# Kernel optimization log

Hardware: AMD Instinct MI355X
Metric: run time of the kernel (lower is better)

Reference implementation:

```python
import jax, jax.numpy as jnp
import numpy as np

B, CIN, COUT, HIN = 2, 64, 64, 96
ALPHA = 0.2       # LeakyReLU slope in GAT
K_RANK = 6        # dist.argsort(1).argsort(1) <= 6  -> 7 nearest neighbors incl. self
DN = ('NCHW', 'OIHW', 'NCHW')


def setup_inputs():
    key = jax.random.key(0)
    ks = jax.random.split(key, 10)
    sc = lambda k, shape, s: jax.random.normal(k, shape, jnp.float32) * s
    return {
        'x': jax.random.normal(ks[0], (B, CIN, HIN, HIN), jnp.float32),
        'conv_w': sc(ks[1], (COUT, CIN, 3, 3), 0.05),
        'conv_b': jnp.zeros((COUT,), jnp.float32),
        'W1': sc(ks[2], (COUT, COUT), 0.1),
        'a1': sc(ks[3], (2 * COUT,), 0.1),
        'W2': sc(ks[4], (COUT, COUT), 0.1),
        'a2': sc(ks[5], (2 * COUT,), 0.1),
        'Wout': sc(ks[6], (2 * COUT, COUT), 0.1),
        'aout': sc(ks[7], (2 * COUT,), 0.1),
        'tconv_w': sc(ks[8], (COUT, COUT, 3, 3), 0.05),  # torch ConvTranspose2d layout [in,out,kh,kw]
        'tconv_b': jnp.zeros((COUT,), jnp.float32),
    }


def _gat_layer(h, adj, W, a, concat):
    # h: [B,N,F_in], W: [F_in,F_out], a: [2*F_out]
    Wh = h @ W                                   # [B,N,F']
    Fo = W.shape[1]
    e = (Wh @ a[:Fo])[:, :, None] + (Wh @ a[Fo:])[:, None, :]   # [B,N,N]
    e = jax.nn.leaky_relu(e, ALPHA)
    e = jnp.where(adj > 0, e, -9e15)
    attn = jax.nn.softmax(e, axis=-1)
    out = jnp.einsum('bij,bjf->bif', attn, Wh)
    return jax.nn.elu(out) if concat else out


def reference(x, conv_w, conv_b, W1, a1, W2, a2, Wout, aout, tconv_w, tconv_b):
    # --- Pre_ProcessLayer_Graph: stride-2 conv, flatten, 7-NN dense adjacency ---
    y = jax.lax.conv_general_dilated(x, conv_w, (2, 2), ((1, 1), (1, 1)),
                                     dimension_numbers=DN) + conv_b[None, :, None, None]
    Bb, C, H, W_ = y.shape
    N = H * W_
    feat = y.reshape(Bb, C, N).transpose(0, 2, 1)          # [B,N,C]
    sq = jnp.sum(feat * feat, axis=-1)                     # [B,N]
    d2 = sq[:, :, None] + sq[:, None, :] - 2.0 * jnp.einsum('bic,bjc->bij', feat, feat)
    dist = jnp.sqrt(jnp.maximum(d2, 0.0))                  # euclidean cdist
    ranks = jnp.argsort(jnp.argsort(dist, axis=-1), axis=-1)
    adj = (ranks <= K_RANK).astype(feat.dtype)             # [B,N,N] binary, incl. self (rank 0)
    # --- GAT (pyGAT style): 2 concat heads + output attention layer, eval mode ---
    h1 = _gat_layer(feat, adj, W1, a1, True)
    h2 = _gat_layer(feat, adj, W2, a2, True)
    hcat = jnp.concatenate([h1, h2], axis=-1)              # [B,N,2C]
    g = jax.nn.elu(_gat_layer(hcat, adj, Wout, aout, False))  # [B,N,C]
    # --- reshape back + transpose conv (k=3, s=2, p=1, output_padding=1) ---
    g = g.transpose(0, 2, 1).reshape(Bb, C, H, W_)
    wt = jnp.flip(tconv_w, (2, 3)).transpose(1, 0, 2, 3)   # -> [out,in,kh,kw]
    out = jax.lax.conv_general_dilated(g, wt, (1, 1), ((1, 2), (1, 2)),
                                       lhs_dilation=(2, 2),
                                       dimension_numbers=DN) + tconv_b[None, :, None, None]
    return out
```

## Files before the change

### kernel.cpp

```cpp
#include <hip/hip_runtime.h>
#include <hip/hip_bf16.h>
#include <stdint.h>

using bf16 = __hip_bfloat16;
using u64 = unsigned long long;

constexpr int B_ = 2;
constexpr int N_ = 2304;

constexpr int OFF_WC2   = 0;
constexpr int OFF_WT2   = 36864;
constexpr int OFF_W1F   = 73728;
constexpr int OFF_W2F   = 77824;
constexpr int OFF_WOUTF = 81920;
constexpr int OFF_A1F   = 90112;
constexpr int OFF_A2F   = 90240;
constexpr int OFF_AOUTF = 90368;
constexpr int OFF_CBF   = 90496;
constexpr int OFF_TBF   = 90560;
constexpr int OFF_FLAG  = 90624;
constexpr int OFF_SQ    = 90688;
constexpr int OFF_S11   = 95296;
constexpr int OFF_S12   = 99904;
constexpr int OFF_S21   = 104512;
constexpr int OFF_S22   = 109120;
constexpr int OFF_S1O   = 113728;
constexpr int OFF_S2O   = 118336;
constexpr int OFF_KNN   = 122944;
constexpr int OFF_BUF0  = 159808;
constexpr int OFF_BUF1  = 454720;
constexpr int OFF_BUF2  = 749632;
constexpr int OFF_BUF3  = 1044544;
constexpr int OFF_PK    = 1339456;

__device__ __forceinline__ float bf2f_raw(unsigned short u) {
    return __uint_as_float(((unsigned int)u) << 16);
}

__device__ __forceinline__ unsigned int mono32(float f) {
    unsigned int u = __float_as_uint(f);
    return (u & 0x80000000u) ? ~u : (u | 0x80000000u);
}

__device__ __forceinline__ bool detect_f32(const void* conv_w) {
    const unsigned short* cw = (const unsigned short*)conv_w;
    float m = 0.f;
    #pragma unroll
    for (int u = 0; u < 64; ++u) {
        float v = fabsf(bf2f_raw(cw[u]));
        if (v < 3.0e38f) m = fmaxf(m, v);
    }
    return m > 1.0e4f;
}

__global__ __launch_bounds__(256) void kc_prep(
    const void* conv_w, const void* conv_b, const void* W1, const void* a1,
    const void* W2, const void* a2, const void* Wout, const void* aout,
    const void* tconv_w, const void* tconv_b, float* __restrict__ ws)
{
    bool f32 = detect_f32(conv_w);
    int idx = blockIdx.x * 256 + threadIdx.x;
    if (idx == 0) ws[OFF_FLAG] = f32 ? 1.f : 0.f;
    if (idx < 32256) ws[OFF_SQ + idx] = 0.f;

    {
        int tap = idx >> 12, ic = (idx >> 6) & 63, oc = idx & 63;
        if (f32) {
            ws[OFF_WC2 + idx] = ((const float*)conv_w)[(oc * 64 + ic) * 9 + tap];
            ws[OFF_WT2 + idx] = ((const float*)tconv_w)[(ic * 64 + oc) * 9 + tap];
        } else {
            ws[OFF_WC2 + idx] = bf2f_raw(((const unsigned short*)conv_w)[(oc * 64 + ic) * 9 + tap]);
            ws[OFF_WT2 + idx] = bf2f_raw(((const unsigned short*)tconv_w)[(ic * 64 + oc) * 9 + tap]);
        }
    }
    if (idx < 4096) {
        if (f32) {
            ws[OFF_W1F + idx] = ((const float*)W1)[idx];
            ws[OFF_W2F + idx] = ((const float*)W2)[idx];
        } else {
            ws[OFF_W1F + idx] = bf2f_raw(((const unsigned short*)W1)[idx]);
            ws[OFF_W2F + idx] = bf2f_raw(((const unsigned short*)W2)[idx]);
        }
    }
    if (idx < 8192)
        ws[OFF_WOUTF + idx] = f32 ? ((const float*)Wout)[idx]
                                  : bf2f_raw(((const unsigned short*)Wout)[idx]);
    if (idx < 128) {
        if (f32) {
            ws[OFF_A1F + idx]   = ((const float*)a1)[idx];
            ws[OFF_A2F + idx]   = ((const float*)a2)[idx];
            ws[OFF_AOUTF + idx] = ((const float*)aout)[idx];
        } else {
            ws[OFF_A1F + idx]   = bf2f_raw(((const unsigned short*)a1)[idx]);
            ws[OFF_A2F + idx]   = bf2f_raw(((const unsigned short*)a2)[idx]);
            ws[OFF_AOUTF + idx] = bf2f_raw(((const unsigned short*)aout)[idx]);
        }
    }
    if (idx < 64) {
        if (f32) {
            ws[OFF_CBF + idx] = ((const float*)conv_b)[idx];
            ws[OFF_TBF + idx] = ((const float*)tconv_b)[idx];
        } else {
            ws[OFF_CBF + idx] = bf2f_raw(((const unsigned short*)conv_b)[idx]);
            ws[OFF_TBF + idx] = bf2f_raw(((const unsigned short*)tconv_b)[idx]);
        }
    }
}

template <bool F32>
__device__ __forceinline__ void conv_body(const void* __restrict__ x,
                                          float* __restrict__ ws,
                                          int n, int ocb, int b)
{
    int oy = n / 48, ox = n - (n / 48) * 48;
    const float* wc2 = ws + OFF_WC2;
    size_t xb = (size_t)b * 64 * 9216;
    float acc[4] = {0, 0, 0, 0};

    for (int ky = 0; ky < 3; ++ky) {
        int iy = 2 * oy - 1 + ky;
        bool vy = (unsigned)iy < 96u;
        int iyc = vy ? iy : 0;
        for (int kx = 0; kx < 3; ++kx) {
            int ix = 2 * ox - 1 + kx;
            bool v = vy && ((unsigned)ix < 96u);
            int ixc = v ? ix : 0;
            size_t xoff = xb + iyc * 96 + ixc;
            const float* wb = wc2 + (ky * 3 + kx) * 4096 + ocb;
            #pragma unroll 8
            for (int ic = 0; ic < 64; ++ic) {
                float xv;
                if (F32) xv = ((const float*)x)[xoff + ic * 9216];
                else     xv = bf2f_raw(((const unsigned short*)x)[xoff + ic * 9216]);
                xv = v ? xv : 0.f;
                const float* wr = wb + ic * 64;
                #pragma unroll
                for (int o = 0; o < 4; ++o) acc[o] += xv * wr[o];
            }
        }
    }
    float* featT = ws + OFF_BUF0 + (size_t)b * 64 * N_;
    const float* cb = ws + OFF_CBF;
    float ssum = 0.f;
    #pragma unroll
    for (int o = 0; o < 4; ++o) {
        float f = acc[o] + cb[ocb + o];
        acc[o] = f;
        featT[(ocb + o) * N_ + n] = f;
        ssum += f * f;
    }
    *(float4*)(ws + OFF_BUF2 + ((size_t)(b * N_ + n) * 64 + ocb)) =
        make_float4(acc[0], acc[1], acc[2], acc[3]);
    atomicAdd(ws + OFF_SQ + b * N_ + n, ssum);
}

__global__ __launch_bounds__(128) void k1_conv(const void* __restrict__ x,
                                               float* __restrict__ ws)
{
    int n   = blockIdx.x * 128 + threadIdx.x;
    int ocb = blockIdx.y * 4;
    int b   = blockIdx.z;
    if (ws[OFF_FLAG] != 0.f) conv_body<true >(x, ws, n, ocb, b);
    else                     conv_body<false>(x, ws, n, ocb, b);
}

__global__ __launch_bounds__(256) void k2_knn(float* __restrict__ ws)
{
    __shared__ float Bs[32][256];
    __shared__ float ys[32][260];
    int tid = threadIdx.x;
    int i0  = blockIdx.x * 32;
    int jh  = blockIdx.y;
    int b   = i0 / N_;
    const float* fT  = ws + OFF_BUF0 + (size_t)b * 64 * N_;
    const float* fnc = ws + OFF_BUF2;
    const float* sq  = ws + OFF_SQ + b * N_;
    int w = tid >> 6, lane = tid & 63;
    int r0 = w * 8;
    int arow0 = __builtin_amdgcn_readfirstlane(i0 + r0);

    u64 K[7];
    #pragma unroll
    for (int t = 0; t < 7; ++t) K[t] = ~0ull;

    int rsel = r0 + (lane >> 3);
    int g    = lane & 7;

    for (int jt = 0; jt < 3; ++jt) {
        int jb = jh * 768 + jt * 256;
        float acc[8][4];
        #pragma unroll
        for (int r = 0; r < 8; ++r)
            #pragma unroll
            for (int c = 0; c < 4; ++c) acc[r][c] = 0.f;

        for (int kh = 0; kh < 2; ++kh) {
            __syncthreads();
            #pragma unroll
            for (int it = 0; it < 8; ++it) {
                int idx = tid + it * 256;
                int k = idx >> 6, j4 = idx & 63;
                float4 v = *(const float4*)(fT + (size_t)(kh * 32 + k) * N_ + jb + j4 * 4);
                *(float4*)&Bs[k][j4 * 4] = v;
            }
            __syncthreads();

            #pragma unroll 2
            for (int k4 = 0; k4 < 8; ++k4) {
                float4 Bv[4];
                #pragma unroll
                for (int kk = 0; kk < 4; ++kk)
                    Bv[kk] = *(const float4*)&Bs[k4 * 4 + kk][4 * lane];
                #pragma unroll
                for (int r = 0; r < 8; ++r) {
                    float4 a = *(const float4*)(fnc + (size_t)(arow0 + r) * 64
                                                + kh * 32 + k4 * 4);
                    acc[r][0] += a.x * Bv[0].x + a.y * Bv[1].x + a.z * Bv[2].x + a.w * Bv[3].x;
                    acc[r][1] += a.x * Bv[0].y + a.y * Bv[1].y + a.z * Bv[2].y + a.w * Bv[3].y;
                    acc[r][2] += a.x * Bv[0].z + a.y * Bv[1].z + a.z * Bv[2].z + a.w * Bv[3].z;
                    acc[r][3] += a.x * Bv[0].w + a.y * Bv[1].w + a.z * Bv[2].w + a.w * Bv[3].w;
                }
            }
        }

        float4 sqv = *(const float4*)(sq + jb + 4 * lane);
        #pragma unroll
        for (int r = 0; r < 8; ++r) {
            float4 yv;
            yv.x = sqv.x - 2.f * acc[r][0];
            yv.y = sqv.y - 2.f * acc[r][1];
            yv.z = sqv.z - 2.f * acc[r][2];
            yv.w = sqv.w - 2.f * acc[r][3];
            *(float4*)&ys[r0 + r][4 * lane] = yv;
        }

        #pragma unroll 8
        for (int u = 0; u < 32; ++u) {
            int jl = g + 8 * u;
            float y = ys[rsel][jl];
            u64 key = ((u64)mono32(y) << 32) | (unsigned int)(jb + jl);
            if (key < K[6]) {
                int pos = 0;
                #pragma unroll
                for (int s = 0; s < 7; ++s) pos += (K[s] < key) ? 1 : 0;
                #pragma unroll
                for (int p = 6; p > 0; --p)
                    K[p] = (p == pos) ? key : ((p > pos) ? K[p - 1] : K[p]);
                if (pos == 0) K[0] = key;
            }
        }
        __syncthreads();
    }

    u64 myk = 0;
    for (int pass = 0; pass < 7; ++pass) {
        u64 m = K[0];
        #pragma unroll
        for (int s = 1; s < 7; ++s) m = (K[s] < m) ? K[s] : m;
        #pragma unroll
        for (int off = 1; off < 8; off <<= 1) {
            u64 o = (u64)__shfl_xor((long long)m, off);
            m = (o < m) ? o : m;
        }
        #pragma unroll
        for (int s = 0; s < 7; ++s)
            if (K[s] == m) K[s] = ~0ull;
        if (g == pass) myk = m;
    }
    if (g < 7) {
        u64* pk = (u64*)(ws + OFF_PK);
        pk[((size_t)(i0 + rsel) * 3 + jh) * 8 + g] = myk;
    }
}

__global__ __launch_bounds__(256) void k_lin(float* __restrict__ ws)
{
    int g = blockIdx.y;
    if (g == 32) {
        int row = blockIdx.x * 256 + threadIdx.x;
        const u64* pk = (const u64*)(ws + OFF_PK) + (size_t)row * 24;
        int* kout = (int*)(ws + OFF_KNN) + (size_t)row * 8;
        u64 L0[7], L1[7], L2[7];
        #pragma unroll
        for (int q = 0; q < 7; ++q) { L0[q] = pk[q]; L1[q] = pk[8 + q]; L2[q] = pk[16 + q]; }
        #pragma unroll
        for (int q = 0; q < 7; ++q) {
            int rank = q;
            #pragma unroll
            for (int p = 0; p < 7; ++p)
                rank += ((L1[p] < L0[q]) ? 1 : 0) + ((L2[p] < L0[q]) ? 1 : 0);
            if (rank < 7) kout[rank] = (int)(L0[q] & 0xffffffffull);
        }
        #pragma unroll
        for (int q = 0; q < 7; ++q) {
            int rank = q;
            #pragma unroll
            for (int p = 0; p < 7; ++p)
                rank += ((L0[p] < L1[q]) ? 1 : 0) + ((L2[p] < L1[q]) ? 1 : 0);
            if (rank < 7) kout[rank] = (int)(L1[q] & 0xffffffffull);
        }
        #pragma unroll
        for (int q = 0; q < 7; ++q) {
            int rank = q;
            #pragma unroll
            for (int p = 0; p < 7; ++p)
                rank += ((L0[p] < L2[q]) ? 1 : 0) + ((L1[p] < L2[q]) ? 1 : 0);
            if (rank < 7) kout[rank] = (int)(L2[q] & 0xffffffffull);
        }
        return;
    }
    int layer = g >> 4;
    int ocb = (g & 15) * 4;
    const float* W  = ws + (layer ? OFF_W2F : OFF_W1F);
    const float* a  = ws + (layer ? OFF_A2F : OFF_A1F);
    float* out_nc   = ws + (layer ? OFF_BUF3 : OFF_BUF1);
    float* s1       = ws + (layer ? OFF_S21 : OFF_S11);
    float* s2       = ws + (layer ? OFF_S22 : OFF_S12);
    int i = blockIdx.x * 256 + threadIdx.x;
    int b = i / N_, n = i - b * N_;
    const float* in_b = ws + OFF_BUF0 + (size_t)b * 64 * N_;

    float acc[4] = {0, 0, 0, 0};
    #pragma unroll 8
    for (int kk = 0; kk < 64; ++kk) {
        float xv = in_b[kk * N_ + n];
        const float* wr = W + kk * 64 + ocb;
        #pragma unroll
        for (int o = 0; o < 4; ++o) acc[o] += xv * wr[o];
    }
    *(float4*)(out_nc + ((size_t)i * 64 + ocb)) =
        make_float4(acc[0], acc[1], acc[2], acc[3]);
    float p1 = 0.f, p2 = 0.f;
    #pragma unroll
    for (int o = 0; o < 4; ++o) {
        p1 += acc[o] * a[ocb + o];
        p2 += acc[o] * a[64 + ocb + o];
    }
    atomicAdd(s1 + i, p1);
    atomicAdd(s2 + i, p2);
}

__global__ __launch_bounds__(256) void k_lin2(float* __restrict__ ws)
{
    int ocb = blockIdx.y * 4;
    int i = blockIdx.x * 256 + threadIdx.x;
    int b = i / N_, n = i - b * N_;
    const float* h1 = ws + OFF_BUF2 + (size_t)b * 64 * N_;
    const float* h2 = ws + OFF_BUF0 + (size_t)b * 64 * N_;
    const float* W  = ws + OFF_WOUTF;
    const float* a  = ws + OFF_AOUTF;

    float acc[4] = {0, 0, 0, 0};
    #pragma unroll 8
    for (int kk = 0; kk < 64; ++kk) {
        float xv = h1[kk * N_ + n];
        const float* wr = W + kk * 64 + ocb;
        #pragma unroll
        for (int o = 0; o < 4; ++o) acc[o] += xv * wr[o];
    }
    #pragma unroll 8
    for (int kk = 0; kk < 64; ++kk) {
        float xv = h2[kk * N_ + n];
        const float* wr = W + (64 + kk) * 64 + ocb;
        #pragma unroll
        for (int o = 0; o < 4; ++o) acc[o] += xv * wr[o];
    }
    *(float4*)(ws + OFF_BUF1 + ((size_t)i * 64 + ocb)) =
        make_float4(acc[0], acc[1], acc[2], acc[3]);
    float p1 = 0.f, p2 = 0.f;
    #pragma unroll
    for (int o = 0; o < 4; ++o) {
        p1 += acc[o] * a[ocb + o];
        p2 += acc[o] * a[64 + ocb + o];
    }
    atomicAdd(ws + OFF_S1O + i, p1);
    atomicAdd(ws + OFF_S2O + i, p2);
}

__device__ __forceinline__ void attn_body(
    const float* __restrict__ Wh_nc, const float* __restrict__ s1,
    const float* __restrict__ s2, const int* __restrict__ knn,
    float* __restrict__ out, int i, int b, int n, int c4)
{
    const int* kp = knn + (size_t)i * 8;
    int j[7];
    #pragma unroll
    for (int t = 0; t < 7; ++t) {
        int jt = kp[t];
        j[t] = ((unsigned)jt < (unsigned)N_) ? jt : 0;
    }
    float si = s1[i];
    const float* s2b = s2 + b * N_;
    float e[7];
    #pragma unroll
    for (int t = 0; t < 7; ++t) {
        float v = si + s2b[j[t]];
        e[t] = v > 0.f ? v : 0.2f * v;
    }
    float m = e[0];
    #pragma unroll
    for (int t = 1; t < 7; ++t) m = fmaxf(m, e[t]);
    float ssum = 0.f;
    #pragma unroll
    for (int t = 0; t < 7; ++t) { e[t] = __expf(e[t] - m); ssum += e[t]; }
    float inv = 1.f / ssum;
    #pragma unroll
    for (int t = 0; t < 7; ++t) e[t] *= inv;

    const float4* W4 = (const float4*)Wh_nc;
    float4 acc = make_float4(0.f, 0.f, 0.f, 0.f);
    #pragma unroll
    for (int t = 0; t < 7; ++t) {
        float4 v = W4[(size_t)(b * N_ + j[t]) * 16 + c4];
        acc.x += e[t] * v.x; acc.y += e[t] * v.y;
        acc.z += e[t] * v.z; acc.w += e[t] * v.w;
    }
    acc.x = acc.x > 0.f ? acc.x : expm1f(acc.x);
    acc.y = acc.y > 0.f ? acc.y : expm1f(acc.y);
    acc.z = acc.z > 0.f ? acc.z : expm1f(acc.z);
    acc.w = acc.w > 0.f ? acc.w : expm1f(acc.w);
    float* ob = out + (size_t)b * 64 * N_;
    ob[(c4 * 4 + 0) * N_ + n] = acc.x;
    ob[(c4 * 4 + 1) * N_ + n] = acc.y;
    ob[(c4 * 4 + 2) * N_ + n] = acc.z;
    ob[(c4 * 4 + 3) * N_ + n] = acc.w;
}

__global__ __launch_bounds__(256) void k_attn12(float* __restrict__ ws)
{
    int layer = blockIdx.z;
    const float* Wh_nc = ws + (layer ? OFF_BUF3 : OFF_BUF1);
    const float* s1    = ws + (layer ? OFF_S21 : OFF_S11);
    const float* s2    = ws + (layer ? OFF_S22 : OFF_S12);
    float* out         = ws + (layer ? OFF_BUF0 : OFF_BUF2);
    int c4 = blockIdx.y;
    int i = blockIdx.x * 256 + threadIdx.x;
    int b = i / N_, n = i - b * N_;
    attn_body(Wh_nc, s1, s2, (const int*)(ws + OFF_KNN), out, i, b, n, c4);
}

__global__ __launch_bounds__(256) void k_attn_out(float* __restrict__ ws)
{
    int c4 = blockIdx.y;
    int i = blockIdx.x * 256 + threadIdx.x;
    int b = i / N_, n = i - b * N_;
    attn_body(ws + OFF_BUF1, ws + OFF_S1O, ws + OFF_S2O,
              (const int*)(ws + OFF_KNN), ws + OFF_BUF3, i, b, n, c4);
}

__global__ __launch_bounds__(128) void k7_tconv(float* __restrict__ ws,
                                                void* __restrict__ outp)
{
    bool f32 = ws[OFF_FLAG] != 0.f;
    int pixc = blockIdx.x * 128 + threadIdx.x;
    int g    = blockIdx.y;
    int pc   = g >> 3, ocb = (g & 7) * 8;
    int b    = blockIdx.z;
    int py = pc >> 1, px = pc & 1;
    int ay = pixc / 48, bx = pixc - (pixc / 48) * 48;
    int oy = 2 * ay + py, ox = 2 * bx + px;

    const float* gT  = ws + OFF_BUF3 + (size_t)b * 64 * N_;
    const float* wt2 = ws + OFF_WT2;
    float acc[8] = {0, 0, 0, 0, 0, 0, 0, 0};

    int nky = py ? 2 : 1;
    int nkx = px ? 2 : 1;
    for (int s = 0; s < nky; ++s) {
        int ky = py ? (s == 0 ? 0 : 2) : 1;
        int iy = py ? (s == 0 ? ay + 1 : ay) : ay;
        bool vy = iy < 48;
        for (int t = 0; t < nkx; ++t) {
            int kx = px ? (t == 0 ? 0 : 2) : 1;
            int ix = px ? (t == 0 ? bx + 1 : bx) : bx;
            bool v = vy && (ix < 48);
            const float* gp = gT + (v ? iy * 48 + ix : 0);
            const float* wb = wt2 + (ky * 3 + kx) * 4096 + ocb;
            #pragma unroll 8
            for (int ic = 0; ic < 64; ++ic) {
                float gv = gp[ic * N_];
                gv = v ? gv : 0.f;
                const float* wr = wb + ic * 64;
                #pragma unroll
                for (int o = 0; o < 8; ++o) acc[o] += gv * wr[o];
            }
        }
    }
    const float* tb = ws + OFF_TBF;
    size_t base = ((size_t)(b * 64 + ocb) * 96 + oy) * 96 + ox;
    if (f32) {
        float* op = (float*)outp;
        #pragma unroll
        for (int o = 0; o < 8; ++o) op[base + (size_t)o * 9216] = acc[o] + tb[ocb + o];
    } else {
        bf16* op = (bf16*)outp;
        #pragma unroll
        for (int o = 0; o < 8; ++o)
            op[base + (size_t)o * 9216] = __float2bfloat16(acc[o] + tb[ocb + o]);
    }
}

extern "C" void kernel_launch(void* const* d_in, const int* in_sizes, int n_in,
                              void* d_out, int out_size, void* d_ws, size_t ws_size,
                              hipStream_t stream)
{
    float* ws = (float*)d_ws;

    hipLaunchKernelGGL(kc_prep, dim3(144), dim3(256), 0, stream,
                       d_in[1], d_in[2], d_in[3], d_in[4], d_in[5], d_in[6],
                       d_in[7], d_in[8], d_in[9], d_in[10], ws);
    hipLaunchKernelGGL(k1_conv, dim3(18, 16, 2), dim3(128), 0, stream, d_in[0], ws);
    hipLaunchKernelGGL(k2_knn, dim3(144, 3), dim3(256), 0, stream, ws);
    hipLaunchKernelGGL(k_lin, dim3(18, 33), dim3(256), 0, stream, ws);
    hipLaunchKernelGGL(k_attn12, dim3(18, 16, 2), dim3(256), 0, stream, ws);
    hipLaunchKernelGGL(k_lin2, dim3(18, 16), dim3(256), 0, stream, ws);
    hipLaunchKernelGGL(k_attn_out, dim3(18, 16), dim3(256), 0, stream, ws);
    hipLaunchKernelGGL(k7_tconv, dim3(18, 32, 2), dim3(128), 0, stream, ws, d_out);
}
```

Baseline: 238.1 us.

## Fuse all stages into one persistent kernel with software grid barriers

Replaces the eight separate kernel launches with a single persistent kernel of 432 blocks. The blocks step through prep, conv, kNN, linear, attention and transposed-conv phases, separated by an atomic-counter grid barrier, and a memset resets the barrier first. This removes per-launch overhead and inter-kernel gaps. It also re-tiles several phases: the kNN y-tile is split into halves so shared memory fits at three blocks per CU, and the attention and tconv phases each handle more channels per thread. In exchange, phases with little work leave blocks idle at barriers, and correctness depends on all 432 blocks being resident at the same time.

```diff
diff --git a/kernel.cpp b/kernel.cpp
--- a/kernel.cpp
+++ b/kernel.cpp
@@ -5,8 +5,9 @@
 using bf16 = __hip_bfloat16;
 using u64 = unsigned long long;
 
-constexpr int B_ = 2;
-constexpr int N_ = 2304;
+constexpr int B_   = 2;
+constexpr int N_   = 2304;
+constexpr int NBLK = 432;
 
 constexpr int OFF_WC2   = 0;
 constexpr int OFF_WT2   = 36864;
@@ -18,7 +19,7 @@
 constexpr int OFF_AOUTF = 90368;
 constexpr int OFF_CBF   = 90496;
 constexpr int OFF_TBF   = 90560;
-constexpr int OFF_FLAG  = 90624;
+constexpr int OFF_BAR   = 90624;
 constexpr int OFF_SQ    = 90688;
 constexpr int OFF_S11   = 95296;
 constexpr int OFF_S12   = 99904;
@@ -53,58 +54,24 @@
     return m > 1.0e4f;
 }
 
-__global__ __launch_bounds__(256) void kc_prep(
-    const void* conv_w, const void* conv_b, const void* W1, const void* a1,
-    const void* W2, const void* a2, const void* Wout, const void* aout,
-    const void* tconv_w, const void* tconv_b, float* __restrict__ ws)
+__device__ __forceinline__ void gbar(int* bar)
 {
-    bool f32 = detect_f32(conv_w);
-    int idx = blockIdx.x * 256 + threadIdx.x;
-    if (idx == 0) ws[OFF_FLAG] = f32 ? 1.f : 0.f;
-    if (idx < 32256) ws[OFF_SQ + idx] = 0.f;
-
-    {
-        int tap = idx >> 12, ic = (idx >> 6) & 63, oc = idx & 63;
-        if (f32) {
-            ws[OFF_WC2 + idx] = ((const float*)conv_w)[(oc * 64 + ic) * 9 + tap];
-            ws[OFF_WT2 + idx] = ((const float*)tconv_w)[(ic * 64 + oc) * 9 + tap];
+    __syncthreads();
+    if (threadIdx.x == 0) {
+        __threadfence();
+        int gen = atomicAdd(&bar[1], 0);
+        int old = atomicAdd(&bar[0], 1);
+        if (old == NBLK - 1) {
+            bar[0] = 0;
+            __threadfence();
+            atomicAdd(&bar[1], 1);
         } else {
-            ws[OFF_WC2 + idx] = bf2f_raw(((const unsigned short*)conv_w)[(oc * 64 + ic) * 9 + tap]);
-            ws[OFF_WT2 + idx] = bf2f_raw(((const unsigned short*)tconv_w)[(ic * 64 + oc) * 9 + tap]);
-        }
-    }
-    if (idx < 4096) {
-        if (f32) {
-            ws[OFF_W1F + idx] = ((const float*)W1)[idx];
-            ws[OFF_W2F + idx] = ((const float*)W2)[idx];
-        } else {
-            ws[OFF_W1F + idx] = bf2f_raw(((const unsigned short*)W1)[idx]);
-            ws[OFF_W2F + idx] = bf2f_raw(((const unsigned short*)W2)[idx]);
-        }
-    }
-    if (idx < 8192)
-        ws[OFF_WOUTF + idx] = f32 ? ((const float*)Wout)[idx]
-                                  : bf2f_raw(((const unsigned short*)Wout)[idx]);
-    if (idx < 128) {
-        if (f32) {
-            ws[OFF_A1F + idx]   = ((const float*)a1)[idx];
-            ws[OFF_A2F + idx]   = ((const float*)a2)[idx];
-            ws[OFF_AOUTF + idx] = ((const float*)aout)[idx];
-        } else {
-            ws[OFF_A1F + idx]   = bf2f_raw(((const unsigned short*)a1)[idx]);
-            ws[OFF_A2F + idx]   = bf2f_raw(((const unsigned short*)a2)[idx]);
-            ws[OFF_AOUTF + idx] = bf2f_raw(((const unsigned short*)aout)[idx]);
-        }
-    }
-    if (idx < 64) {
-        if (f32) {
-            ws[OFF_CBF + idx] = ((const float*)conv_b)[idx];
-            ws[OFF_TBF + idx] = ((const float*)tconv_b)[idx];
-        } else {
-            ws[OFF_CBF + idx] = bf2f_raw(((const unsigned short*)conv_b)[idx]);
-            ws[OFF_TBF + idx] = bf2f_raw(((const unsigned short*)tconv_b)[idx]);
-        }
-    }
+            while (atomicAdd(&bar[1], 0) == gen)
+                __builtin_amdgcn_s_sleep(8);
+        }
+        __threadfence();
+    }
+    __syncthreads();
 }
 
 template <bool F32>
@@ -154,130 +121,278 @@
     atomicAdd(ws + OFF_SQ + b * N_ + n, ssum);
 }
 
-__global__ __launch_bounds__(128) void k1_conv(const void* __restrict__ x,
-                                               float* __restrict__ ws)
+__device__ __forceinline__ void attn_body8(
+    const float* __restrict__ Wh_nc, const float* __restrict__ s1,
+    const float* __restrict__ s2, const int* __restrict__ knn,
+    float* __restrict__ out, int i, int b, int n, int c8)
 {
-    int n   = blockIdx.x * 128 + threadIdx.x;
-    int ocb = blockIdx.y * 4;
-    int b   = blockIdx.z;
-    if (ws[OFF_FLAG] != 0.f) conv_body<true >(x, ws, n, ocb, b);
-    else                     conv_body<false>(x, ws, n, ocb, b);
-}
-
-__global__ __launch_bounds__(256) void k2_knn(float* __restrict__ ws)
+    const int* kp = knn + (size_t)i * 8;
+    int j[7];
+    #pragma unroll
+    for (int t = 0; t < 7; ++t) {
+        int jt = kp[t];
+        j[t] = ((unsigned)jt < (unsigned)N_) ? jt : 0;
+    }
+    float si = s1[i];
+    const float* s2b = s2 + b * N_;
+    float e[7];
+    #pragma unroll
+    for (int t = 0; t < 7; ++t) {
+        float v = si + s2b[j[t]];
+        e[t] = v > 0.f ? v : 0.2f * v;
+    }
+    float m = e[0];
+    #pragma unroll
+    for (int t = 1; t < 7; ++t) m = fmaxf(m, e[t]);
+    float ssum = 0.f;
+    #pragma unroll
+    for (int t = 0; t < 7; ++t) { e[t] = __expf(e[t] - m); ssum += e[t]; }
+    float inv = 1.f / ssum;
+    #pragma unroll
+    for (int t = 0; t < 7; ++t) e[t] *= inv;
+
+    const float4* W4 = (const float4*)Wh_nc;
+    float* ob = out + (size_t)b * 64 * N_;
+    #pragma unroll
+    for (int q = 0; q < 2; ++q) {
+        int c4 = c8 * 2 + q;
+        float4 acc = make_float4(0.f, 0.f, 0.f, 0.f);
+        #pragma unroll
+        for (int t = 0; t < 7; ++t) {
+            float4 v = W4[(size_t)(b * N_ + j[t]) * 16 + c4];
+            acc.x += e[t] * v.x; acc.y += e[t] * v.y;
+            acc.z += e[t] * v.z; acc.w += e[t] * v.w;
+        }
+        acc.x = acc.x > 0.f ? acc.x : expm1f(acc.x);
+        acc.y = acc.y > 0.f ? acc.y : expm1f(acc.y);
+        acc.z = acc.z > 0.f ? acc.z : expm1f(acc.z);
+        acc.w = acc.w > 0.f ? acc.w : expm1f(acc.w);
+        ob[(c4 * 4 + 0) * N_ + n] = acc.x;
+        ob[(c4 * 4 + 1) * N_ + n] = acc.y;
+        ob[(c4 * 4 + 2) * N_ + n] = acc.z;
+        ob[(c4 * 4 + 3) * N_ + n] = acc.w;
+    }
+}
+
+__global__ __launch_bounds__(256, 3) void mega(
+    const void* __restrict__ x,
+    const void* conv_w, const void* conv_b, const void* W1, const void* a1,
+    const void* W2, const void* a2, const void* Wout, const void* aout,
+    const void* tconv_w, const void* tconv_b,
+    float* __restrict__ ws, void* __restrict__ outp)
 {
-    __shared__ float Bs[32][256];
-    __shared__ float ys[32][260];
+    __shared__ __align__(16) float smemf[12416];
     int tid = threadIdx.x;
-    int i0  = blockIdx.x * 32;
-    int jh  = blockIdx.y;
-    int b   = i0 / N_;
-    const float* fT  = ws + OFF_BUF0 + (size_t)b * 64 * N_;
-    const float* fnc = ws + OFF_BUF2;
-    const float* sq  = ws + OFF_SQ + b * N_;
-    int w = tid >> 6, lane = tid & 63;
-    int r0 = w * 8;
-    int arow0 = __builtin_amdgcn_readfirstlane(i0 + r0);
-
-    u64 K[7];
-    #pragma unroll
-    for (int t = 0; t < 7; ++t) K[t] = ~0ull;
-
-    int rsel = r0 + (lane >> 3);
-    int g    = lane & 7;
-
-    for (int jt = 0; jt < 3; ++jt) {
-        int jb = jh * 768 + jt * 256;
-        float acc[8][4];
-        #pragma unroll
-        for (int r = 0; r < 8; ++r)
-            #pragma unroll
-            for (int c = 0; c < 4; ++c) acc[r][c] = 0.f;
-
-        for (int kh = 0; kh < 2; ++kh) {
-            __syncthreads();
-            #pragma unroll
-            for (int it = 0; it < 8; ++it) {
-                int idx = tid + it * 256;
-                int k = idx >> 6, j4 = idx & 63;
-                float4 v = *(const float4*)(fT + (size_t)(kh * 32 + k) * N_ + jb + j4 * 4);
-                *(float4*)&Bs[k][j4 * 4] = v;
-            }
-            __syncthreads();
-
-            #pragma unroll 2
-            for (int k4 = 0; k4 < 8; ++k4) {
-                float4 Bv[4];
+    int bid = blockIdx.x;
+    int gid = bid * 256 + tid;
+    int* bar = (int*)(ws + OFF_BAR);
+    bool f32 = detect_f32(conv_w);
+
+    {
+        int idx = gid;
+        if (idx < 32256) ws[OFF_SQ + idx] = 0.f;
+        if (idx < 36864) {
+            int tap = idx >> 12, ic = (idx >> 6) & 63, oc = idx & 63;
+            if (f32) {
+                ws[OFF_WC2 + idx] = ((const float*)conv_w)[(oc * 64 + ic) * 9 + tap];
+                ws[OFF_WT2 + idx] = ((const float*)tconv_w)[(ic * 64 + oc) * 9 + tap];
+            } else {
+                ws[OFF_WC2 + idx] = bf2f_raw(((const unsigned short*)conv_w)[(oc * 64 + ic) * 9 + tap]);
+                ws[OFF_WT2 + idx] = bf2f_raw(((const unsigned short*)tconv_w)[(ic * 64 + oc) * 9 + tap]);
+            }
+            if (idx < 4096) {
+                if (f32) {
+                    ws[OFF_W1F + idx] = ((const float*)W1)[idx];
+                    ws[OFF_W2F + idx] = ((const float*)W2)[idx];
+                } else {
+                    ws[OFF_W1F + idx] = bf2f_raw(((const unsigned short*)W1)[idx]);
+                    ws[OFF_W2F + idx] = bf2f_raw(((const unsigned short*)W2)[idx]);
+                }
+            }
+            if (idx < 8192)
+                ws[OFF_WOUTF + idx] = f32 ? ((const float*)Wout)[idx]
+                                          : bf2f_raw(((const unsigned short*)Wout)[idx]);
+            if (idx < 128) {
+                if (f32) {
+                    ws[OFF_A1F + idx]   = ((const float*)a1)[idx];
+                    ws[OFF_A2F + idx]   = ((const float*)a2)[idx];
+                    ws[OFF_AOUTF + idx] = ((const float*)aout)[idx];
+                } else {
+                    ws[OFF_A1F + idx]   = bf2f_raw(((const unsigned short*)a1)[idx]);
+                    ws[OFF_A2F + idx]   = bf2f_raw(((const unsigned short*)a2)[idx]);
+                    ws[OFF_AOUTF + idx] = bf2f_raw(((const unsigned short*)aout)[idx]);
+                }
+            }
+            if (idx < 64) {
+                if (f32) {
+                    ws[OFF_CBF + idx] = ((const float*)conv_b)[idx];
+                    ws[OFF_TBF + idx] = ((const float*)tconv_b)[idx];
+                } else {
+                    ws[OFF_CBF + idx] = bf2f_raw(((const unsigned short*)conv_b)[idx]);
+                    ws[OFF_TBF + idx] = bf2f_raw(((const unsigned short*)tconv_b)[idx]);
+                }
+            }
+        }
+    }
+    gbar(bar);
+
+    if (gid < 73728) {
+        int n = gid % 2304;
+        int r = gid / 2304;
+        int ocb = (r & 15) * 4;
+        int b = r >> 4;
+        if (f32) conv_body<true >(x, ws, n, ocb, b);
+        else     conv_body<false>(x, ws, n, ocb, b);
+    }
+    gbar(bar);
+
+    {
+        float* Bs = smemf;
+        float* ys = smemf + 8192;
+        int i0 = (bid / 3) * 32;
+        int jh = bid % 3;
+        int b2 = i0 / N_;
+        const float* fT  = ws + OFF_BUF0 + (size_t)b2 * 64 * N_;
+        const float* fnc = ws + OFF_BUF2;
+        const float* sq  = ws + OFF_SQ + b2 * N_;
+        int w = tid >> 6, lane = tid & 63;
+        int r0 = w * 8;
+        int arow0 = __builtin_amdgcn_readfirstlane(i0 + r0);
+
+        u64 K[7];
+        #pragma unroll
+        for (int t = 0; t < 7; ++t) K[t] = ~0ull;
+        int rsel = r0 + (lane >> 3);
+        int g = lane & 7;
+
+        for (int jt = 0; jt < 3; ++jt) {
+            int jb = jh * 768 + jt * 256;
+            float acc[8][4];
+            #pragma unroll
+            for (int r = 0; r < 8; ++r)
                 #pragma unroll
-                for (int kk = 0; kk < 4; ++kk)
-                    Bv[kk] = *(const float4*)&Bs[k4 * 4 + kk][4 * lane];
+                for (int c = 0; c < 4; ++c) acc[r][c] = 0.f;
+
+            for (int kh = 0; kh < 2; ++kh) {
+                __syncthreads();
                 #pragma unroll
-                for (int r = 0; r < 8; ++r) {
-                    float4 a = *(const float4*)(fnc + (size_t)(arow0 + r) * 64
-                                                + kh * 32 + k4 * 4);
-                    acc[r][0] += a.x * Bv[0].x + a.y * Bv[1].x + a.z * Bv[2].x + a.w * Bv[3].x;
-                    acc[r][1] += a.x * Bv[0].y + a.y * Bv[1].y + a.z * Bv[2].y + a.w * Bv[3].y;
-                    acc[r][2] += a.x * Bv[0].z + a.y * Bv[1].z + a.z * Bv[2].z + a.w * Bv[3].z;
-                    acc[r][3] += a.x * Bv[0].w + a.y * Bv[1].w + a.z * Bv[2].w + a.w * Bv[3].w;
-                }
-            }
-        }
-
-        float4 sqv = *(const float4*)(sq + jb + 4 * lane);
-        #pragma unroll
-        for (int r = 0; r < 8; ++r) {
-            float4 yv;
-            yv.x = sqv.x - 2.f * acc[r][0];
-            yv.y = sqv.y - 2.f * acc[r][1];
-            yv.z = sqv.z - 2.f * acc[r][2];
-            yv.w = sqv.w - 2.f * acc[r][3];
-            *(float4*)&ys[r0 + r][4 * lane] = yv;
-        }
-
+                for (int it = 0; it < 8; ++it) {
+                    int idx = tid + it * 256;
+                    int k = idx >> 6, j4 = idx & 63;
+                    float4 v = *(const float4*)(fT + (size_t)(kh * 32 + k) * N_ + jb + j4 * 4);
+                    *(float4*)&Bs[k * 256 + j4 * 4] = v;
+                }
+                __syncthreads();
+
+                #pragma unroll 2
+                for (int k4 = 0; k4 < 8; ++k4) {
+                    float4 Bv[4];
+                    #pragma unroll
+                    for (int kk = 0; kk < 4; ++kk)
+                        Bv[kk] = *(const float4*)&Bs[(k4 * 4 + kk) * 256 + 4 * lane];
+                    #pragma unroll
+                    for (int r = 0; r < 8; ++r) {
+                        float4 a = *(const float4*)(fnc + (size_t)(arow0 + r) * 64
+                                                    + kh * 32 + k4 * 4);
+                        acc[r][0] += a.x * Bv[0].x + a.y * Bv[1].x + a.z * Bv[2].x + a.w * Bv[3].x;
+                        acc[r][1] += a.x * Bv[0].y + a.y * Bv[1].y + a.z * Bv[2].y + a.w * Bv[3].y;
+                        acc[r][2] += a.x * Bv[0].z + a.y * Bv[1].z + a.z * Bv[2].z + a.w * Bv[3].z;
+                        acc[r][3] += a.x * Bv[0].w + a.y * Bv[1].w + a.z * Bv[2].w + a.w * Bv[3].w;
+                    }
+                }
+            }
+
+            float4 sqv = *(const float4*)(sq + jb + 4 * lane);
+            #pragma unroll
+            for (int hf = 0; hf < 2; ++hf) {
+                __syncthreads();
+                if ((lane >> 5) == hf) {
+                    int col = 4 * (lane & 31);
+                    #pragma unroll
+                    for (int r = 0; r < 8; ++r) {
+                        float4 yv;
+                        yv.x = sqv.x - 2.f * acc[r][0];
+                        yv.y = sqv.y - 2.f * acc[r][1];
+                        yv.z = sqv.z - 2.f * acc[r][2];
+                        yv.w = sqv.w - 2.f * acc[r][3];
+                        *(float4*)&ys[(r0 + r) * 132 + col] = yv;
+                    }
+                }
+                __syncthreads();
+                #pragma unroll 4
+                for (int u = 0; u < 16; ++u) {
+                    int jl = g + 8 * u;
+                    float y = ys[rsel * 132 + jl];
+                    u64 key = ((u64)mono32(y) << 32) | (unsigned int)(jb + 128 * hf + jl);
+                    if (key < K[6]) {
+                        int pos = 0;
+                        #pragma unroll
+                        for (int s = 0; s < 7; ++s) pos += (K[s] < key) ? 1 : 0;
+                        #pragma unroll
+                        for (int p = 6; p > 0; --p)
+                            K[p] = (p == pos) ? key : ((p > pos) ? K[p - 1] : K[p]);
+                        if (pos == 0) K[0] = key;
+                    }
+                }
+            }
+        }
+
+        u64 myk = 0;
+        for (int pass = 0; pass < 7; ++pass) {
+            u64 m = K[0];
+            #pragma unroll
+            for (int s = 1; s < 7; ++s) m = (K[s] < m) ? K[s] : m;
+            #pragma unroll
+            for (int off = 1; off < 8; off <<= 1) {
+                u64 o = (u64)__shfl_xor((long long)m, off);
+                m = (o < m) ? o : m;
+            }
+            #pragma unroll
+            for (int s = 0; s < 7; ++s)
+                if (K[s] == m) K[s] = ~0ull;
+            if (g == pass) myk = m;
+        }
+        if (g < 7) {
+            u64* pk = (u64*)(ws + OFF_PK);
+            pk[((size_t)(i0 + rsel) * 3 + jh) * 8 + g] = myk;
+        }
+    }
+    gbar(bar);
+
+    if (gid < 73728) {
+        int i = gid % 4608;
+        int gq = gid / 4608;
+        int layer = gq >> 3;
+        int ocb = (gq & 7) * 8;
+        const float* W  = ws + (layer ? OFF_W2F : OFF_W1F);
+        const float* a  = ws + (layer ? OFF_A2F : OFF_A1F);
+        float* out_nc   = ws + (layer ? OFF_BUF3 : OFF_BUF1);
+        float* s1       = ws + (layer ? OFF_S21 : OFF_S11);
+        float* s2       = ws + (layer ? OFF_S22 : OFF_S12);
+        int b = i / N_, n = i - b * N_;
+        const float* in_b = ws + OFF_BUF0 + (size_t)b * 64 * N_;
+
+        float acc[8] = {0, 0, 0, 0, 0, 0, 0, 0};
         #pragma unroll 8
-        for (int u = 0; u < 32; ++u) {
-            int jl = g + 8 * u;
-            float y = ys[rsel][jl];
-            u64 key = ((u64)mono32(y) << 32) | (unsigned int)(jb + jl);
-            if (key < K[6]) {
-                int pos = 0;
-                #pragma unroll
-                for (int s = 0; s < 7; ++s) pos += (K[s] < key) ? 1 : 0;
-                #pragma unroll
-                for (int p = 6; p > 0; --p)
-                    K[p] = (p == pos) ? key : ((p > pos) ? K[p - 1] : K[p]);
-                if (pos == 0) K[0] = key;
-            }
-        }
-        __syncthreads();
-    }
-
-    u64 myk = 0;
-    for (int pass = 0; pass < 7; ++pass) {
-        u64 m = K[0];
-        #pragma unroll
-        for (int s = 1; s < 7; ++s) m = (K[s] < m) ? K[s] : m;
-        #pragma unroll
-        for (int off = 1; off < 8; off <<= 1) {
-            u64 o = (u64)__shfl_xor((long long)m, off);
-            m = (o < m) ? o : m;
-        }
-        #pragma unroll
-        for (int s = 0; s < 7; ++s)
-            if (K[s] == m) K[s] = ~0ull;
-        if (g == pass) myk = m;
-    }
-    if (g < 7) {
-        u64* pk = (u64*)(ws + OFF_PK);
-        pk[((size_t)(i0 + rsel) * 3 + jh) * 8 + g] = myk;
-    }
-}
-
-__global__ __launch_bounds__(256) void k_lin(float* __restrict__ ws)
-{
-    int g = blockIdx.y;
-    if (g == 32) {
-        int row = blockIdx.x * 256 + threadIdx.x;
+        for (int kk = 0; kk < 64; ++kk) {
+            float xv = in_b[kk * N_ + n];
+            const float* wr = W + kk * 64 + ocb;
+            #pragma unroll
+            for (int o = 0; o < 8; ++o) acc[o] += xv * wr[o];
+        }
+        float4* ob = (float4*)(out_nc + ((size_t)i * 64 + ocb));
+        ob[0] = make_float4(acc[0], acc[1], acc[2], acc[3]);
+        ob[1] = make_float4(acc[4], acc[5], acc[6], acc[7]);
+        float p1 = 0.f, p2 = 0.f;
+        #pragma unroll
+        for (int o = 0; o < 8; ++o) {
+            p1 += acc[o] * a[ocb + o];
+            p2 += acc[o] * a[64 + ocb + o];
+        }
+        atomicAdd(s1 + i, p1);
+        atomicAdd(s2 + i, p2);
+    } else if (gid < 78336) {
+        int row = gid - 73728;
         const u64* pk = (const u64*)(ws + OFF_PK) + (size_t)row * 24;
         int* kout = (int*)(ws + OFF_KNN) + (size_t)row * 8;
         u64 L0[7], L1[7], L2[7];
@@ -307,196 +422,121 @@
                 rank += ((L0[p] < L2[q]) ? 1 : 0) + ((L1[p] < L2[q]) ? 1 : 0);
             if (rank < 7) kout[rank] = (int)(L2[q] & 0xffffffffull);
         }
-        return;
-    }
-    int layer = g >> 4;
-    int ocb = (g & 15) * 4;
-    const float* W  = ws + (layer ? OFF_W2F : OFF_W1F);
-    const float* a  = ws + (layer ? OFF_A2F : OFF_A1F);
-    float* out_nc   = ws + (layer ? OFF_BUF3 : OFF_BUF1);
-    float* s1       = ws + (layer ? OFF_S21 : OFF_S11);
-    float* s2       = ws + (layer ? OFF_S22 : OFF_S12);
-    int i = blockIdx.x * 256 + threadIdx.x;
-    int b = i / N_, n = i - b * N_;
-    const float* in_b = ws + OFF_BUF0 + (size_t)b * 64 * N_;
-
-    float acc[4] = {0, 0, 0, 0};
-    #pragma unroll 8
-    for (int kk = 0; kk < 64; ++kk) {
-        float xv = in_b[kk * N_ + n];
-        const float* wr = W + kk * 64 + ocb;
-        #pragma unroll
-        for (int o = 0; o < 4; ++o) acc[o] += xv * wr[o];
-    }
-    *(float4*)(out_nc + ((size_t)i * 64 + ocb)) =
-        make_float4(acc[0], acc[1], acc[2], acc[3]);
-    float p1 = 0.f, p2 = 0.f;
-    #pragma unroll
-    for (int o = 0; o < 4; ++o) {
-        p1 += acc[o] * a[ocb + o];
-        p2 += acc[o] * a[64 + ocb + o];
-    }
-    atomicAdd(s1 + i, p1);
-    atomicAdd(s2 + i, p2);
-}
-
-__global__ __launch_bounds__(256) void k_lin2(float* __restrict__ ws)
-{
-    int ocb = blockIdx.y * 4;
-    int i = blockIdx.x * 256 + threadIdx.x;
-    int b = i / N_, n = i - b * N_;
-    const float* h1 = ws + OFF_BUF2 + (size_t)b * 64 * N_;
-    const float* h2 = ws + OFF_BUF0 + (size_t)b * 64 * N_;
-    const float* W  = ws + OFF_WOUTF;
-    const float* a  = ws + OFF_AOUTF;
-
-    float acc[4] = {0, 0, 0, 0};
-    #pragma unroll 8
-    for (int kk = 0; kk < 64; ++kk) {
-        float xv = h1[kk * N_ + n];
-        const float* wr = W + kk * 64 + ocb;
-        #pragma unroll
-        for (int o = 0; o < 4; ++o) acc[o] += xv * wr[o];
-    }
-    #pragma unroll 8
-    for (int kk = 0; kk < 64; ++kk) {
-        float xv = h2[kk * N_ + n];
-        const float* wr = W + (64 + kk) * 64 + ocb;
-        #pragma unroll
-        for (int o = 0; o < 4; ++o) acc[o] += xv * wr[o];
-    }
-    *(float4*)(ws + OFF_BUF1 + ((size_t)i * 64 + ocb)) =
-        make_float4(acc[0], acc[1], acc[2], acc[3]);
-    float p1 = 0.f, p2 = 0.f;
-    #pragma unroll
-    for (int o = 0; o < 4; ++o) {
-        p1 += acc[o] * a[ocb + o];
-        p2 += acc[o] * a[64 + ocb + o];
-    }
-    atomicAdd(ws + OFF_S1O + i, p1);
-    atomicAdd(ws + OFF_S2O + i, p2);
-}
-
-__device__ __forceinline__ void attn_body(
-    const float* __restrict__ Wh_nc, const float* __restrict__ s1,
-    const float* __restrict__ s2, const int* __restrict__ knn,
-    float* __restrict__ out, int i, int b, int n, int c4)
-{
-    const int* kp = knn + (size_t)i * 8;
-    int j[7];
-    #pragma unroll
-    for (int t = 0; t < 7; ++t) {
-        int jt = kp[t];
-        j[t] = ((unsigned)jt < (unsigned)N_) ? jt : 0;
-    }
-    float si = s1[i];
-    const float* s2b = s2 + b * N_;
-    float e[7];
-    #pragma unroll
-    for (int t = 0; t < 7; ++t) {
-        float v = si + s2b[j[t]];
-        e[t] = v > 0.f ? v : 0.2f * v;
-    }
-    float m = e[0];
-    #pragma unroll
-    for (int t = 1; t < 7; ++t) m = fmaxf(m, e[t]);
-    float ssum = 0.f;
-    #pragma unroll
-    for (int t = 0; t < 7; ++t) { e[t] = __expf(e[t] - m); ssum += e[t]; }
-    float inv = 1.f / ssum;
-    #pragma unroll
-    for (int t = 0; t < 7; ++t) e[t] *= inv;
-
-    const float4* W4 = (const float4*)Wh_nc;
-    float4 acc = make_float4(0.f, 0.f, 0.f, 0.f);
-    #pragma unroll
-    for (int t = 0; t < 7; ++t) {
-        float4 v = W4[(size_t)(b * N_ + j[t]) * 16 + c4];
-        acc.x += e[t] * v.x; acc.y += e[t] * v.y;
-        acc.z += e[t] * v.z; acc.w += e[t] * v.w;
-    }
-    acc.x = acc.x > 0.f ? acc.x : expm1f(acc.x);
-    acc.y = acc.y > 0.f ? acc.y : expm1f(acc.y);
-    acc.z = acc.z > 0.f ? acc.z : expm1f(acc.z);
-    acc.w = acc.w > 0.f ? acc.w : expm1f(acc.w);
-    float* ob = out + (size_t)b * 64 * N_;
-    ob[(c4 * 4 + 0) * N_ + n] = acc.x;
-    ob[(c4 * 4 + 1) * N_ + n] = acc.y;
-    ob[(c4 * 4 + 2) * N_ + n] = acc.z;
-    ob[(c4 * 4 + 3) * N_ + n] = acc.w;
-}
-
-__global__ __launch_bounds__(256) void k_attn12(float* __restrict__ ws)
-{
-    int layer = blockIdx.z;
-    const float* Wh_nc = ws + (layer ? OFF_BUF3 : OFF_BUF1);
-    const float* s1    = ws + (layer ? OFF_S21 : OFF_S11);
-    const float* s2    = ws + (layer ? OFF_S22 : OFF_S12);
-    float* out         = ws + (layer ? OFF_BUF0 : OFF_BUF2);
-    int c4 = blockIdx.y;
-    int i = blockIdx.x * 256 + threadIdx.x;
-    int b = i / N_, n = i - b * N_;
-    attn_body(Wh_nc, s1, s2, (const int*)(ws + OFF_KNN), out, i, b, n, c4);
-}
-
-__global__ __launch_bounds__(256) void k_attn_out(float* __restrict__ ws)
-{
-    int c4 = blockIdx.y;
-    int i = blockIdx.x * 256 + threadIdx.x;
-    int b = i / N_, n = i - b * N_;
-    attn_body(ws + OFF_BUF1, ws + OFF_S1O, ws + OFF_S2O,
-              (const int*)(ws + OFF_KNN), ws + OFF_BUF3, i, b, n, c4);
-}
-
-__global__ __launch_bounds__(128) void k7_tconv(float* __restrict__ ws,
-                                                void* __restrict__ outp)
-{
-    bool f32 = ws[OFF_FLAG] != 0.f;
-    int pixc = blockIdx.x * 128 + threadIdx.x;
-    int g    = blockIdx.y;
-    int pc   = g >> 3, ocb = (g & 7) * 8;
-    int b    = blockIdx.z;
-    int py = pc >> 1, px = pc & 1;
-    int ay = pixc / 48, bx = pixc - (pixc / 48) * 48;
-    int oy = 2 * ay + py, ox = 2 * bx + px;
-
-    const float* gT  = ws + OFF_BUF3 + (size_t)b * 64 * N_;
-    const float* wt2 = ws + OFF_WT2;
-    float acc[8] = {0, 0, 0, 0, 0, 0, 0, 0};
-
-    int nky = py ? 2 : 1;
-    int nkx = px ? 2 : 1;
-    for (int s = 0; s < nky; ++s) {
-        int ky = py ? (s == 0 ? 0 : 2) : 1;
-        int iy = py ? (s == 0 ? ay + 1 : ay) : ay;
-        bool vy = iy < 48;
-        for (int t = 0; t < nkx; ++t) {
-            int kx = px ? (t == 0 ? 0 : 2) : 1;
-            int ix = px ? (t == 0 ? bx + 1 : bx) : bx;
-            bool v = vy && (ix < 48);
-            const float* gp = gT + (v ? iy * 48 + ix : 0);
-            const float* wb = wt2 + (ky * 3 + kx) * 4096 + ocb;
-            #pragma unroll 8
-            for (int ic = 0; ic < 64; ++ic) {
-                float gv = gp[ic * N_];
-                gv = v ? gv : 0.f;
-                const float* wr = wb + ic * 64;
-                #pragma unroll
-                for (int o = 0; o < 8; ++o) acc[o] += gv * wr[o];
-            }
-        }
-    }
-    const float* tb = ws + OFF_TBF;
-    size_t base = ((size_t)(b * 64 + ocb) * 96 + oy) * 96 + ox;
-    if (f32) {
-        float* op = (float*)outp;
-        #pragma unroll
-        for (int o = 0; o < 8; ++o) op[base + (size_t)o * 9216] = acc[o] + tb[ocb + o];
-    } else {
-        bf16* op = (bf16*)outp;
-        #pragma unroll
-        for (int o = 0; o < 8; ++o)
-            op[base + (size_t)o * 9216] = __float2bfloat16(acc[o] + tb[ocb + o]);
+    }
+    gbar(bar);
+
+    if (gid < 73728) {
+        int i = gid % 4608;
+        int gq = gid / 4608;
+        int layer = gq >> 3;
+        int c8 = gq & 7;
+        const float* Wh_nc = ws + (layer ? OFF_BUF3 : OFF_BUF1);
+        const float* s1    = ws + (layer ? OFF_S21 : OFF_S11);
+        const float* s2    = ws + (layer ? OFF_S22 : OFF_S12);
+        float* out         = ws + (layer ? OFF_BUF0 : OFF_BUF2);
+        int b = i / N_, n = i - b * N_;
+        attn_body8(Wh_nc, s1, s2, (const int*)(ws + OFF_KNN), out, i, b, n, c8);
+    }
+    gbar(bar);
+
+    if (gid < 36864) {
+        int i = gid % 4608;
+        int ocb = (gid / 4608) * 8;
+        int b = i / N_, n = i - b * N_;
+        const float* h1 = ws + OFF_BUF2 + (size_t)b * 64 * N_;
+        const float* h2 = ws + OFF_BUF0 + (size_t)b * 64 * N_;
+        const float* W  = ws + OFF_WOUTF;
+        const float* a  = ws + OFF_AOUTF;
+
+        float acc[8] = {0, 0, 0, 0, 0, 0, 0, 0};
+        #pragma unroll 8
+        for (int kk = 0; kk < 64; ++kk) {
+            float xv = h1[kk * N_ + n];
+            const float* wr = W + kk * 64 + ocb;
+            #pragma unroll
+            for (int o = 0; o < 8; ++o) acc[o] += xv * wr[o];
+        }
+        #pragma unroll 8
+        for (int kk = 0; kk < 64; ++kk) {
+            float xv = h2[kk * N_ + n];
+            const float* wr = W + (64 + kk) * 64 + ocb;
+            #pragma unroll
+            for (int o = 0; o < 8; ++o) acc[o] += xv * wr[o];
+        }
+        float4* ob = (float4*)(ws + OFF_BUF1 + ((size_t)i * 64 + ocb));
+        ob[0] = make_float4(acc[0], acc[1], acc[2], acc[3]);
+        ob[1] = make_float4(acc[4], acc[5], acc[6], acc[7]);
+        float p1 = 0.f, p2 = 0.f;
+        #pragma unroll
+        for (int o = 0; o < 8; ++o) {
+            p1 += acc[o] * a[ocb + o];
+            p2 += acc[o] * a[64 + ocb + o];
+        }
+        atomicAdd(ws + OFF_S1O + i, p1);
+        atomicAdd(ws + OFF_S2O + i, p2);
+    }
+    gbar(bar);
+
+    if (gid < 36864) {
+        int i = gid % 4608;
+        int c8 = gid / 4608;
+        int b = i / N_, n = i - b * N_;
+        attn_body8(ws + OFF_BUF1, ws + OFF_S1O, ws + OFF_S2O,
+                   (const int*)(ws + OFF_KNN), ws + OFF_BUF3, i, b, n, c8);
+    }
+    gbar(bar);
+
+    if (gid < 73728) {
+        int pixc = gid % 2304;
+        int gq = gid / 2304;
+        int b = gq >> 4;
+        int rem = gq & 15;
+        int pc = rem >> 2;
+        int ocb = (rem & 3) * 16;
+        int py = pc >> 1, px = pc & 1;
+        int ay = pixc / 48, bx = pixc - (pixc / 48) * 48;
+        int oy = 2 * ay + py, ox = 2 * bx + px;
+
+        const float* gT  = ws + OFF_BUF3 + (size_t)b * 64 * N_;
+        const float* wt2 = ws + OFF_WT2;
+        float acc[16];
+        #pragma unroll
+        for (int o = 0; o < 16; ++o) acc[o] = 0.f;
+
+        int nky = py ? 2 : 1;
+        int nkx = px ? 2 : 1;
+        for (int s = 0; s < nky; ++s) {
+            int ky = py ? (s == 0 ? 0 : 2) : 1;
+            int iy = py ? (s == 0 ? ay + 1 : ay) : ay;
+            bool vy = iy < 48;
+            for (int t = 0; t < nkx; ++t) {
+                int kx = px ? (t == 0 ? 0 : 2) : 1;
+                int ix = px ? (t == 0 ? bx + 1 : bx) : bx;
+                bool v = vy && (ix < 48);
+                const float* gp = gT + (v ? iy * 48 + ix : 0);
+                const float* wb = wt2 + (ky * 3 + kx) * 4096 + ocb;
+                #pragma unroll 8
+                for (int ic = 0; ic < 64; ++ic) {
+                    float gv = gp[ic * N_];
+                    gv = v ? gv : 0.f;
+                    const float* wr = wb + ic * 64;
+                    #pragma unroll
+                    for (int o = 0; o < 16; ++o) acc[o] += gv * wr[o];
+                }
+            }
+        }
+        const float* tb = ws + OFF_TBF;
+        size_t base = ((size_t)(b * 64 + ocb) * 96 + oy) * 96 + ox;
+        if (f32) {
+            float* op = (float*)outp;
+            #pragma unroll
+            for (int o = 0; o < 16; ++o) op[base + (size_t)o * 9216] = acc[o] + tb[ocb + o];
+        } else {
+            bf16* op = (bf16*)outp;
+            #pragma unroll
+            for (int o = 0; o < 16; ++o)
+                op[base + (size_t)o * 9216] = __float2bfloat16(acc[o] + tb[ocb + o]);
+        }
     }
 }
 
@@ -505,15 +545,9 @@
                               hipStream_t stream)
 {
     float* ws = (float*)d_ws;
-
-    hipLaunchKernelGGL(kc_prep, dim3(144), dim3(256), 0, stream,
-                       d_in[1], d_in[2], d_in[3], d_in[4], d_in[5], d_in[6],
-                       d_in[7], d_in[8], d_in[9], d_in[10], ws);
-    hipLaunchKernelGGL(k1_conv, dim3(18, 16, 2), dim3(128), 0, stream, d_in[0], ws);
-    hipLaunchKernelGGL(k2_knn, dim3(144, 3), dim3(256), 0, stream, ws);
-    hipLaunchKernelGGL(k_lin, dim3(18, 33), dim3(256), 0, stream, ws);
-    hipLaunchKernelGGL(k_attn12, dim3(18, 16, 2), dim3(256), 0, stream, ws);
-    hipLaunchKernelGGL(k_lin2, dim3(18, 16), dim3(256), 0, stream, ws);
-    hipLaunchKernelGGL(k_attn_out, dim3(18, 16), dim3(256), 0, stream, ws);
-    hipLaunchKernelGGL(k7_tconv, dim3(18, 32, 2), dim3(128), 0, stream, ws, d_out);
-}
+    hipMemsetAsync((char*)d_ws + (size_t)OFF_BAR * 4, 0, 64, stream);
+    hipLaunchKernelGGL(mega, dim3(NBLK), dim3(256), 0, stream,
+                       d_in[0], d_in[1], d_in[2], d_in[3], d_in[4], d_in[5],
+                       d_in[6], d_in[7], d_in[8], d_in[9], d_in[10],
+                       ws, d_out);
+}
```

New measurement: 661.9 us. 2.78x slower.
